# Performance work log

Measured on AMD Instinct MI355X. Metric: run time of the kernel, lower is better.

## Reference

```python
import jax, jax.numpy as jnp
import numpy as np
from jax import lax

C_LIGHT = 3e8
SPATIAL, CROP = 64, 128
BIN_LEN, WALL, SAMP_COEFF, CYCLES = 0.01, 2.0, 2.0, 5
B, D = 2, 1


def _waveconvparam(bin_resolution, virtual_wavelength, cycles):
    samples = int(round(cycles * virtual_wavelength / (C_LIGHT * bin_resolution)))
    num_cycles = samples * (C_LIGHT * bin_resolution) / virtual_wavelength
    sigma = 0.3
    g = np.arange(samples, dtype=np.float64)
    env = np.exp(-(((g - samples / 2.0) / (samples / 2.0)) ** 2) / (2 * sigma ** 2))
    cos_k = np.cos(2 * np.pi * num_cycles * g / samples) * env
    sin_k = np.sin(2 * np.pi * num_cycles * g / samples) * env
    return cos_k, sin_k


def _define_psf(N, M, slope):
    # LCT psf: locus of min |(4 slope)^2 (x^2+y^2) - z|, normalized and circularly shifted
    x = np.arange(2 * N, dtype=np.float64) / (2 * N - 1) * 2 - 1
    z = np.arange(2 * M, dtype=np.float64) / (2 * M - 1) * 2
    gy, gx, gz = np.meshgrid(x, x, z)  # (2N,2N,2M)
    blur = np.abs((4 * slope) ** 2 * (gx ** 2 + gy ** 2) - gz)
    d = (np.abs(blur - blur.min(axis=2, keepdims=True)) < 1e-8).astype(np.float64)
    e = d / np.sqrt(d.sum())
    f = np.roll(np.roll(e, N, axis=0), N, axis=1)
    return np.transpose(f, (2, 0, 1))  # (2M,2N,2N)


def _resampling_operator(M):
    row = M * M
    x = np.arange(1, row + 1, dtype=np.float64)
    mtx = np.zeros((row, M), dtype=np.float64)
    mtx[np.arange(row), np.ceil(np.sqrt(x)).astype(np.int64) - 1] = 1.0
    mtx = mtx / np.sqrt(x)[:, None]
    mtxi = mtx.T.copy()
    for _ in range(int(np.log2(M))):
        mtx = 0.5 * (mtx[0::2] + mtx[1::2])
        mtxi = 0.5 * (mtxi[:, 0::2] + mtxi[:, 1::2])
    return mtx.astype(np.float32), mtxi.astype(np.float32)


def setup_inputs() -> dict:
    key = jax.random.key(0)
    kf, kw, kb = jax.random.split(key, 3)
    bin_res = BIN_LEN / C_LIGHT
    trange = CROP * C_LIGHT * bin_res
    slope = (WALL / 2.0) / trange
    vlam = SAMP_COEFF * 2.0 * (WALL / (SPATIAL - 1))
    cos_k, sin_k = _waveconvparam(bin_res, vlam, CYCLES)
    wave = np.stack([cos_k, sin_k], 0)[:, ::-1][:, None, :].astype(np.float32)  # (2,1,k)
    psf = _define_psf(SPATIAL, CROP, slope)
    invpsf = np.conj(np.fft.fftn(psf))
    mtx, mtxi = _resampling_operator(CROP)
    return {
        "feature": jax.random.normal(kf, (B, D, CROP, SPATIAL, SPATIAL), jnp.float32),
        "conv_w": jax.random.normal(kw, ()) * 0.1 + 1.0,
        "conv_b": jax.random.normal(kb, ()) * 0.1,
        "wave": jnp.asarray(wave),
        "invpsf_real": jnp.asarray(np.real(invpsf).astype(np.float32))[None],
        "invpsf_imag": jnp.asarray(np.imag(invpsf).astype(np.float32))[None],
        "mtx": jnp.asarray(mtx),
        "mtxi": jnp.asarray(mtxi),
    }


def _attention(k1, k2, w, b):
    # SE-style cross attention; Conv3d(1,1,1) on unbatched (C=1,T,H,W) is w*x+b
    T = k2.shape[1]
    pe = jnp.sin(jnp.arange(T, dtype=k2.dtype))  # PE3D with 1 channel -> sin along T
    k2p = k2 + pe[None, :, None, None]
    scal = jnp.mean(w * k1 + b)  # conv + adaptive_avg_pool3d(1), channel dim = 1
    q = (w * k2p + b).reshape(1, 1, -1)
    attn = jax.nn.sigmoid(jax.nn.softmax(scal * q, axis=2)).reshape(k2p.shape)
    return attn * k2p


def _fre_atten2(kernel, w, b):
    _, T, H, W = kernel.shape
    ct, ch, cw = T // 2, H // 2, W // 2
    st, sh, sw = (T - ct) // 2, (H - ch) // 2, (W - cw) // 2
    sl = (slice(None), slice(ct - st, ct + st), slice(ch - sh, ch + sh), slice(cw - sw, cw + sw))
    high = kernel[sl]
    low = jnp.roll(kernel, (ct, ch, cw), axis=(1, 2, 3))[sl]
    l2l = _attention(low, low, w, b)
    l2h = _attention(l2l, high, w, b)
    temp = kernel.at[sl].set(l2h)
    temp = jnp.roll(temp, (ct, ch, cw), axis=(1, 2, 3)).at[sl].set(l2l)
    return jnp.roll(temp, (ct, ch, cw), axis=(1, 2, 3))


def _forward(feature, conv_w, conv_b, wave, invpsf_real, invpsf_imag, mtx, mtxi):
    b, d, T, H, W = feature.shape
    BD = b * d
    k = wave.shape[2]
    # virtual wave conv along time: (BDHW,1,T) x (2,1,k)
    data = feature.reshape(BD, T, H, W).transpose(0, 2, 3, 1).reshape(-1, 1, T)
    conv = lax.conv_general_dilated(data, wave, (1,), [(k // 2, k // 2)],
                                    dimension_numbers=("NCH", "OIH", "NCH"))
    if k % 2 == 0:
        conv = conv[:, :, 1:]
    data2 = conv.reshape(BD, H, W, 2, T).transpose(3, 0, 4, 1, 2).reshape(2 * BD, T, H, W)
    # temporal resampling then zero-pad to 2T,2H,2W
    tmp = jnp.einsum("tm,bmx->btx", mtx, data2.reshape(2 * BD, T, H * W)).reshape(2 * BD, T, H, W)
    datapad = jnp.zeros((2 * BD, 2 * T, 2 * H, 2 * W), feature.dtype).at[:, :T, :H, :W].set(tmp)
    datafre = jnp.fft.fftn(datapad)  # torch.fft.fftn transforms ALL dims incl. batch
    w1 = _fre_atten2(invpsf_real, conv_w, conv_b)
    w2 = _fre_atten2(invpsf_imag, conv_w, conv_b)
    re_real = datafre.real * w1 - datafre.imag * w2
    re_imag = datafre.real * w2 + datafre.imag * w1
    re = jnp.fft.ifftn(lax.complex(re_real, re_imag))
    vol = re[:, :T, :H, :W]
    cr, ci = vol[:BD].real, vol[:BD].imag
    sr, si = vol[BD:].real, vol[BD:].imag
    sum_real = cr ** 2 - ci ** 2 + sr ** 2 - si ** 2
    sum_imag = 2 * cr * ci + 2 * sr * si
    mag = jax.nn.relu((jnp.sqrt(sum_real ** 2 + sum_imag ** 2) + sum_real) * 0.5)
    sq = jnp.sqrt(mag)
    out = jnp.einsum("tm,bmx->btx", mtxi, sq.reshape(BD, T, H * W))
    return out.reshape(b, d, T, H, W)


def reference(feature, conv_w, conv_b, wave, invpsf_real, invpsf_imag, mtx, mtxi):
    return _forward(feature, conv_w, conv_b, wave, invpsf_real, invpsf_imag, mtx, mtxi)
```

## Files before the change

kernel.cpp:

```cpp
#include <hip/hip_runtime.h>

#define BLKE 524288
#define VOLE 4194304
#define TCROP 2097152
#define PI2 6.283185307179586476925286766559

__device__ __forceinline__ float2 cmulf(float2 a, float2 b){
  return make_float2(a.x*b.x - a.y*b.y, a.x*b.y + a.y*b.x);
}
__device__ __forceinline__ float waveSum(float v){
  #pragma unroll
  for (int o=32;o;o>>=1) v += __shfl_xor(v,o);
  return v;
}
__device__ __forceinline__ float waveMaxf(float v){
  #pragma unroll
  for (int o=32;o;o>>=1) v = fmaxf(v,__shfl_xor(v,o));
  return v;
}
__device__ __forceinline__ float waveMinf(float v){
  #pragma unroll
  for (int o=32;o;o>>=1) v = fminf(v,__shfl_xor(v,o));
  return v;
}

__device__ __forceinline__ void bcastReduce5(const float* __restrict__ pA, int kap,
    float& sum, float& mnl, float& mxl, float& mnh, float& mxh, float* sm ){
  int tid = threadIdx.x;
  const float* q = pA + kap*1280 + tid*5;
  float s = q[0], a = q[1], b = q[2], c = q[3], d = q[4];
  s = waveSum(s); a = waveMinf(a); b = waveMaxf(b); c = waveMinf(c); d = waveMaxf(d);
  if ((tid&63)==0){ int w = tid>>6; sm[w]=s; sm[4+w]=a; sm[8+w]=b; sm[12+w]=c; sm[16+w]=d; }
  __syncthreads();
  sum = sm[0]+sm[1]+sm[2]+sm[3];
  mnl = fminf(fminf(sm[4],sm[5]),fminf(sm[6],sm[7]));
  mxl = fmaxf(fmaxf(sm[8],sm[9]),fmaxf(sm[10],sm[11]));
  mnh = fminf(fminf(sm[12],sm[13]),fminf(sm[14],sm[15]));
  mxh = fmaxf(fmaxf(sm[16],sm[17]),fmaxf(sm[18],sm[19]));
}

__device__ __forceinline__ float bcastSum256(const float* __restrict__ p, float* sm ){
  int tid = threadIdx.x;
  float s = waveSum(p[tid]);
  if ((tid&63)==0) sm[tid>>6] = s;
  __syncthreads();
  return sm[0]+sm[1]+sm[2]+sm[3];
}

__global__ void __launch_bounds__(256) kD1(const float* __restrict__ mtx,
                                           const float* __restrict__ wave,
                                           float* __restrict__ M,
                                           const float* __restrict__ Kr,
                                           const float* __restrict__ Ki,
                                           float* __restrict__ Lw, float* __restrict__ Hw,
                                           float* __restrict__ pA){
  __shared__ float spe[128];
  __shared__ float sm[20];
  int bid = blockIdx.x;
  int tid = threadIdx.x;
  if (bid < 512){
    int kap = bid >> 8, bx = bid & 255;
    const float* K = kap ? Ki : Kr;
    if (tid < 128) spe[tid] = sinf((float)tid);
    __syncthreads();
    float sum=0.f, mnl=3.4e38f, mxl=-3.4e38f, mnh=3.4e38f, mxh=-3.4e38f;
    int base = bx*256 + tid;
    #pragma unroll
    for (int it = 0; it < 8; it++){
      int e = base + it*65536;
      int tau = e >> 12, rem = e & 4095, eta = rem >> 6, om = rem & 63;
      float pe = spe[tau];
      float lo = K[(size_t)((tau+192)&255)*16384 + ((eta+96)&127)*128 + ((om+96)&127)];
      float hi = K[(size_t)(tau+64)*16384 + (eta+32)*128 + (om+32)];
      sum += lo;
      float lp = lo+pe, hp = hi+pe;
      Lw[kap*BLKE + e] = lp;
      Hw[kap*BLKE + e] = hp;
      mnl=fminf(mnl,lp); mxl=fmaxf(mxl,lp);
      mnh=fminf(mnh,hp); mxh=fmaxf(mxh,hp);
    }
    sum = waveSum(sum); mnl=waveMinf(mnl); mxl=waveMaxf(mxl); mnh=waveMinf(mnh); mxh=waveMaxf(mxh);
    if ((tid&63)==0){ int w=tid>>6; sm[w]=sum; sm[4+w]=mnl; sm[8+w]=mxl; sm[12+w]=mnh; sm[16+w]=mxh; }
    __syncthreads();
    if (tid==0){
      float* o = pA + kap*1280 + bx*5;
      o[0] = sm[0]+sm[1]+sm[2]+sm[3];
      o[1] = fminf(fminf(sm[4],sm[5]),fminf(sm[6],sm[7]));
      o[2] = fmaxf(fmaxf(sm[8],sm[9]),fmaxf(sm[10],sm[11]));
      o[3] = fminf(fminf(sm[12],sm[13]),fminf(sm[14],sm[15]));
      o[4] = fmaxf(fmaxf(sm[16],sm[17]),fmaxf(sm[18],sm[19]));
    }
  } else {
    int idx = (bid-512)*256 + tid;
    int o = idx >> 14, r = idx & 16383;
    int t = r >> 7, s = r & 127;
    float acc = 0.f;
    int mlo = s-31; if (mlo < 0) mlo = 0;
    int mhi = s+31; if (mhi > 127) mhi = 127;
    for (int m = mlo; m <= mhi; m++) acc += mtx[t*128+m]*wave[o*63 + (s-m+31)];
    M[idx] = acc;
  }
}

__global__ void __launch_bounds__(256) kD2(const float* __restrict__ feat,
                                           const float* __restrict__ M,
                                           float* __restrict__ tmp,
                                           const float* __restrict__ pA,
                                           const float* __restrict__ Lw,
                                           float* __restrict__ pB,
                                           const float* cw, const float* cb){
  __shared__ __align__(16) char smem[16640];
  __shared__ float sm[20], smo[4];
  int bid = blockIdx.x;
  int tid = threadIdx.x;
  if (bid < 512){
    int kap = bid >> 8, bx = bid & 255;
    float sum,mnl,mxl,mnh,mxh;
    bcastReduce5(pA,kap,sum,mnl,mxl,mnh,mxh,sm);
    float w = cw[0], b = cb[0];
    float s1 = w*(sum*(1.0f/BLKE)) + b;
    float a1 = s1*w, c1 = s1*b;
    float mx = (a1>=0.f) ? a1*mxl+c1 : a1*mnl+c1;
    float acc = 0.f;
    int base = kap*BLKE + bx*256 + tid;
    #pragma unroll
    for (int it = 0; it < 8; it++){
      float lp = Lw[base + it*65536];
      acc += expf(a1*lp + c1 - mx);
    }
    acc = waveSum(acc);
    if ((tid&63)==0) smo[tid>>6] = acc;
    __syncthreads();
    if (tid==0) pB[kap*256 + bx] = smo[0]+smo[1]+smo[2]+smo[3];
  } else {
    int e = bid - 512;
    int b = e >> 8, tt = (e >> 6) & 3, xt = e & 63;
    float (*LF)[64] = (float(*)[64])smem;
    float (*LM)[32][33] = (float(*)[32][33])(smem + 8192);
    int xx = tid & 63, tq = tid >> 6;
    float acc0[8] = {}, acc1[8] = {};
    const float* fb = feat + (size_t)b*BLKE;
    for (int sb = 0; sb < 4; sb++){
      #pragma unroll
      for (int j = 0; j < 8; j++){
        int idx = tid + j*256; int s = idx >> 6, x = idx & 63;
        LF[s][x] = fb[(size_t)(sb*32+s)*4096 + xt*64 + x];
      }
      #pragma unroll
      for (int j = 0; j < 8; j++){
        int idx = tid + j*256; int o = idx >> 10, r = idx & 1023;
        int trow = r >> 5, s = r & 31;
        LM[o][trow][s] = M[o*16384 + (tt*32+trow)*128 + sb*32+s];
      }
      __syncthreads();
      for (int s = 0; s < 32; s++){
        float f = LF[s][xx];
        #pragma unroll
        for (int i = 0; i < 8; i++){
          acc0[i] += LM[0][tq*8+i][s]*f;
          acc1[i] += LM[1][tq*8+i][s]*f;
        }
      }
      __syncthreads();
    }
    #pragma unroll
    for (int i = 0; i < 8; i++){
      int t = tt*32 + tq*8 + i;
      tmp[(size_t)(0*2+b)*BLKE + (size_t)t*4096 + xt*64+xx] = acc0[i];
      tmp[(size_t)(1*2+b)*BLKE + (size_t)t*4096 + xt*64+xx] = acc1[i];
    }
  }
}

__global__ void __launch_bounds__(256) kD3(const float* __restrict__ tmp,
                                           float2* __restrict__ Z2,
                                           const float* __restrict__ pA,
                                           const float* __restrict__ pB,
                                           const float* __restrict__ Lw,
                                           float* __restrict__ pC,
                                           const float* cw, const float* cb){
  __shared__ __align__(16) char smem[8832];
  __shared__ float sm[20], smB[4], smo[4];
  int bid = blockIdx.x;
  int tid = threadIdx.x;
  if (bid < 512){
    int kap = bid >> 8, bx = bid & 255;
    float sum,mnl,mxl,mnh,mxh;
    bcastReduce5(pA,kap,sum,mnl,mxl,mnh,mxh,sm);
    float d1 = bcastSum256(pB + kap*256, smB);
    float w = cw[0], b = cb[0];
    float s1 = w*(sum*(1.0f/BLKE)) + b;
    float a1 = s1*w, c1 = s1*b;
    float mx = (a1>=0.f) ? a1*mxl+c1 : a1*mnl+c1;
    float invd = 1.0f/d1;
    float acc = 0.f;
    int base = kap*BLKE + bx*256 + tid;
    #pragma unroll
    for (int it = 0; it < 8; it++){
      float lp = Lw[base + it*65536];
      float p = expf(a1*lp + c1 - mx)*invd;
      acc += lp/(1.f + expf(-p));
    }
    acc = waveSum(acc);
    if ((tid&63)==0) smo[tid>>6] = acc;
    __syncthreads();
    if (tid==0) pC[kap*256 + bx] = smo[0]+smo[1]+smo[2]+smo[3];
  } else {
    int e = bid - 512;
    int b = e >> 11, bx = e & 2047;
    float2 (*bA)[130] = (float2(*)[130])smem;
    float2 (*bB)[130] = (float2(*)[130])(smem + 4160);
    float2* tw = (float2*)(smem + 8320);
    if (tid < 64){
      double ang = -PI2 * (double)tid / 128.0;
      tw[tid] = make_float2((float)cos(ang), (float)sin(ang));
    }
    int l = tid >> 6, lane = tid & 63;
    int line = bx*4 + l;
    int t = line >> 6, h = line & 63;
    const float* pc = tmp + (size_t)b*BLKE + (size_t)t*4096 + h*64;
    const float* ps = tmp + (size_t)(2+b)*BLKE + (size_t)t*4096 + h*64;
    bA[l][lane] = make_float2(pc[lane], ps[lane]);
    bA[l][lane+64] = make_float2(0.f, 0.f);
    __syncthreads();
    float2 (*src)[130] = bA, (*dst)[130] = bB;
    int m = 1;
    #pragma unroll
    for (int st = 0; st < 7; st++){
      int i = lane;
      int jm = i & ~(m-1);
      float2 a = src[l][i], b2 = src[l][i+64];
      float2 s = make_float2(a.x+b2.x, a.y+b2.y);
      float2 d = make_float2(a.x-b2.x, a.y-b2.y);
      dst[l][i+jm]   = s;
      dst[l][i+jm+m] = cmulf(d, tw[jm]);
      __syncthreads();
      float2 (*tp)[130] = src; src = dst; dst = tp;
      m <<= 1;
    }
    float2* outp = Z2 + (size_t)b*TCROP + (size_t)t*16384 + (size_t)h*128;
    outp[lane]    = src[l][lane];
    outp[lane+64] = src[l][lane+64];
  }
}

__global__ void __launch_bounds__(256) kD4(float2* __restrict__ Z2,
                                           const float* __restrict__ pA,
                                           const float* __restrict__ pC,
                                           const float* __restrict__ Hw,
                                           float* __restrict__ pD,
                                           const float* cw, const float* cb){
  __shared__ __align__(16) char smem[33792];
  __shared__ float sm[20], smC[4], smo[4];
  int bid = blockIdx.x;
  int tid = threadIdx.x;
  if (bid < 512){
    int kap = bid >> 8, bx = bid & 255;
    float sum,mnl,mxl,mnh,mxh;
    bcastReduce5(pA,kap,sum,mnl,mxl,mnh,mxh,sm);
    float sl2 = bcastSum256(pC + kap*256, smC);
    float w = cw[0], b = cb[0];
    float s2 = w*(sl2*(1.0f/BLKE)) + b;
    float a2 = s2*w, c2 = s2*b;
    float mx = (a2>=0.f) ? a2*mxh+c2 : a2*mnh+c2;
    float acc = 0.f;
    int base = kap*BLKE + bx*256 + tid;
    #pragma unroll
    for (int it = 0; it < 8; it++){
      float hp = Hw[base + it*65536];
      acc += expf(a2*hp + c2 - mx);
    }
    acc = waveSum(acc);
    if ((tid&63)==0) smo[tid>>6] = acc;
    __syncthreads();
    if (tid==0) pD[kap*256 + bx] = smo[0]+smo[1]+smo[2]+smo[3];
  } else {
    int e = bid - 512;
    int b = e >> 10, bx = e & 1023;
    float2 (*bA)[130] = (float2(*)[130])smem;
    float2 (*bB)[130] = (float2(*)[130])(smem + 16640);
    float2* tw = (float2*)(smem + 33280);
    if (tid < 64){
      double ang = -PI2 * (double)tid / 128.0;
      tw[tid] = make_float2((float)cos(ang), (float)sin(ang));
    }
    float2* Z = Z2 + (size_t)b*TCROP;
    int t = bx >> 3; int w0 = (bx & 7) << 4;
    size_t base = (size_t)t*16384 + w0;
    #pragma unroll
    for (int q = 0; q < 4; q++){
      int idx = q*256 + tid; int wl = idx & 15, hh = idx >> 4;
      bA[wl][hh] = Z[base + (size_t)hh*128 + wl];
      bA[wl][hh+64] = make_float2(0.f, 0.f);
    }
    __syncthreads();
    float2 (*src)[130] = bA, (*dst)[130] = bB;
    int m = 1;
    #pragma unroll
    for (int st = 0; st < 7; st++){
      #pragma unroll
      for (int q = 0; q < 4; q++){
        int g = q*256 + tid; int li = g >> 6; int i = g & 63;
        int jm = i & ~(m-1);
        float2 a = src[li][i], b2 = src[li][i+64];
        float2 s = make_float2(a.x+b2.x, a.y+b2.y);
        float2 d = make_float2(a.x-b2.x, a.y-b2.y);
        dst[li][i+jm]   = s;
        dst[li][i+jm+m] = cmulf(d, tw[jm]);
      }
      __syncthreads();
      float2 (*tp)[130] = src; src = dst; dst = tp;
      m <<= 1;
    }
    #pragma unroll
    for (int q = 0; q < 8; q++){
      int idx = q*256 + tid; int wl = idx & 15, hh = idx >> 4;
      Z[base + (size_t)hh*128 + wl] = src[wl][hh];
    }
  }
}

__device__ __forceinline__ float attnv(float v, float a, float c, float mx, float invd){
  float p = expf(a*v + c - mx)*invd;
  return v / (1.f + expf(-p));
}
__device__ __forceinline__ float2 wcAt(int t, int h, int w,
                                       const float* __restrict__ Kr, const float* __restrict__ Ki,
                                       const float* spe, const float* P){
  size_t off = (size_t)t*16384 + (size_t)h*128 + w;
  float kr = Kr[off], ki = Ki[off];
  bool center = (t>=64 && t<192) && (h>=32 && h<96) && (w>=32 && w<96);
  int tc = (t+64)&255, hc = (h+32)&127, wc = (w+32)&127;
  bool corner = (tc<128) && (hc<64) && (wc<64);
  float2 o;
  if (center){
    float pe = spe[t-64];
    o.x = attnv(kr+pe, P[4],  P[5],  P[6],  P[7]);
    o.y = attnv(ki+pe, P[12], P[13], P[14], P[15]);
  } else if (corner){
    float pe = spe[tc];
    o.x = attnv(kr+pe, P[0], P[1],  P[2],  P[3]);
    o.y = attnv(ki+pe, P[8], P[9],  P[10], P[11]);
  } else {
    o.x = kr; o.y = ki;
  }
  return o;
}

__global__ void __launch_bounds__(256) kWcF(const float* __restrict__ Kr,
                                            const float* __restrict__ Ki,
                                            const float* __restrict__ pA,
                                            const float* __restrict__ pB,
                                            const float* __restrict__ pC,
                                            const float* __restrict__ pD,
                                            const float* cw, const float* cb,
                                            float2* __restrict__ Wc){
  __shared__ float spe[128];
  __shared__ float P[16];
  __shared__ float sm[20], smB[4], smC[4], smD[4];
  int tid = threadIdx.x;
  if (tid < 128) spe[tid] = sinf((float)tid);
  for (int kap = 0; kap < 2; kap++){
    if (kap) __syncthreads();
    float sum,mnl,mxl,mnh,mxh;
    bcastReduce5(pA,kap,sum,mnl,mxl,mnh,mxh,sm);
    float d1  = bcastSum256(pB + kap*256, smB);
    float sl2 = bcastSum256(pC + kap*256, smC);
    float d2  = bcastSum256(pD + kap*256, smD);
    if (tid==0){
      float w = cw[0], b = cb[0];
      float s1 = w*(sum*(1.0f/BLKE)) + b;
      float a1 = s1*w, c1 = s1*b;
      float mx1 = (a1>=0.f) ? a1*mxl+c1 : a1*mnl+c1;
      float s2 = w*(sl2*(1.0f/BLKE)) + b;
      float a2 = s2*w, c2 = s2*b;
      float mx2 = (a2>=0.f) ? a2*mxh+c2 : a2*mnh+c2;
      float* Q = P + kap*8;
      Q[0]=a1; Q[1]=c1; Q[2]=mx1; Q[3]=1.0f/d1;
      Q[4]=a2; Q[5]=c2; Q[6]=mx2; Q[7]=1.0f/d2;
    }
  }
  __syncthreads();
  #pragma unroll
  for (int q = 0; q < 4; q++){
    int idx = blockIdx.x*1024 + q*256 + tid;
    int t = idx >> 14, r = idx & 16383, h = r >> 7, w = r & 127;
    Wc[idx] = wcAt(t, h, w, Kr, Ki, spe, P);
  }
}

__global__ void __launch_bounds__(256) kTfused(const float2* __restrict__ Z2,
                                               float2* __restrict__ U2,
                                               float2* __restrict__ V2,
                                               const float2* __restrict__ Wc){
  __shared__ float2 buf[16][259];
  __shared__ float2 tw[256];
  int tid = threadIdx.x;
  {
    double ang = -PI2 * (double)tid / 256.0;
    tw[tid] = make_float2((float)cos(ang), (float)sin(ang));
  }
  int b = blockIdx.y;
  int bid = blockIdx.x;
  int h = bid >> 3, w0 = (bid & 7) << 4;
  int wl = tid & 15, pq = tid >> 4;
  const float2* Z = Z2 + (size_t)b*TCROP;
  size_t gbase = (size_t)h*128 + w0 + wl;
  #pragma unroll
  for (int q = 0; q < 8; q++){
    int p = q*16 + pq;
    buf[wl][p] = Z[(size_t)p*16384 + gbase];
    buf[wl][p+128] = make_float2(0.f, 0.f);
  }
  __syncthreads();
  #pragma unroll
  for (int st = 0; st < 4; st++){
    const int Q = 64 >> (2*st);
    const int f = 1 << (2*st);
    #pragma unroll
    for (int it = 0; it < 4; it++){
      int u = pq + 16*it;
      int j = u & (Q-1);
      int seg = u >> (6 - 2*st);
      int base = (seg << (8 - 2*st)) + j;
      float2 a0 = buf[wl][base];
      float2 a1 = buf[wl][base+Q];
      float2 a2 = buf[wl][base+2*Q];
      float2 a3 = buf[wl][base+3*Q];
      float2 t0 = make_float2(a0.x+a2.x, a0.y+a2.y);
      float2 t1 = make_float2(a0.x-a2.x, a0.y-a2.y);
      float2 t2 = make_float2(a1.x+a3.x, a1.y+a3.y);
      float2 t3 = make_float2(a1.x-a3.x, a1.y-a3.y);
      float2 z0 = make_float2(t0.x+t2.x, t0.y+t2.y);
      float2 z2 = make_float2(t0.x-t2.x, t0.y-t2.y);
      float2 z1 = make_float2(t1.x+t3.y, t1.y-t3.x);
      float2 z3 = make_float2(t1.x-t3.y, t1.y+t3.x);
      buf[wl][base]     = z0;
      buf[wl][base+Q]   = cmulf(z1, tw[f*j]);
      buf[wl][base+2*Q] = cmulf(z2, tw[2*f*j]);
      buf[wl][base+3*Q] = cmulf(z3, tw[3*f*j]);
    }
    __syncthreads();
  }
  float2 rg[16];
  #pragma unroll
  for (int q = 0; q < 16; q++) rg[q] = buf[wl][q*16 + pq];
  #pragma unroll
  for (int q = 0; q < 16; q++){
    int p = q*16 + pq;
    int kt = ((p&3)<<6) | (((p>>2)&3)<<4) | (((p>>4)&3)<<2) | ((p>>6)&3);
    float2 wc = Wc[(size_t)kt*16384 + (size_t)h*128 + w0 + wl];
    buf[wl][p] = cmulf(rg[q], wc);
  }
  __syncthreads();
  #pragma unroll
  for (int st = 0; st < 4; st++){
    const int Q = 1 << (2*st);
    const int f = 64 >> (2*st);
    #pragma unroll
    for (int it = 0; it < 4; it++){
      int u = pq + 16*it;
      int j = u & (Q-1);
      int seg = u >> (2*st);
      int base = (seg << (2*st + 2)) + j;
      float2 w1 = tw[f*j], w2 = tw[2*f*j], w3 = tw[3*f*j];
      float2 a0 = buf[wl][base];
      float2 r1 = buf[wl][base+Q];
      float2 r2 = buf[wl][base+2*Q];
      float2 r3 = buf[wl][base+3*Q];
      float2 b1 = make_float2(r1.x*w1.x + r1.y*w1.y, r1.y*w1.x - r1.x*w1.y);
      float2 b2 = make_float2(r2.x*w2.x + r2.y*w2.y, r2.y*w2.x - r2.x*w2.y);
      float2 b3 = make_float2(r3.x*w3.x + r3.y*w3.y, r3.y*w3.x - r3.x*w3.y);
      float2 t0 = make_float2(a0.x+b2.x, a0.y+b2.y);
      float2 t1 = make_float2(a0.x-b2.x, a0.y-b2.y);
      float2 t2 = make_float2(b1.x+b3.x, b1.y+b3.y);
      float2 t3 = make_float2(b1.x-b3.x, b1.y-b3.y);
      buf[wl][base]     = make_float2(t0.x+t2.x, t0.y+t2.y);
      buf[wl][base+Q]   = make_float2(t1.x-t3.y, t1.y+t3.x);
      buf[wl][base+2*Q] = make_float2(t0.x-t2.x, t0.y-t2.y);
      buf[wl][base+3*Q] = make_float2(t1.x+t3.y, t1.y-t3.x);
    }
    __syncthreads();
  }
  float2* Uo = U2 + (size_t)b*TCROP;
  #pragma unroll
  for (int q = 0; q < 8; q++){
    int p = q*16 + pq;
    Uo[(size_t)p*16384 + gbase] = buf[wl][p];
  }
  #pragma unroll
  for (int q = 0; q < 16; q++){
    int p = q*16 + pq;
    int kt = ((p&3)<<6) | (((p>>2)&3)<<4) | (((p>>4)&3)<<2) | ((p>>6)&3);
    int tm = (256-kt)&255, hm = (128-h)&127, wm = (128-(w0+wl))&127;
    float2 wc = Wc[(size_t)tm*16384 + (size_t)hm*128 + wm];
    wc.y = -wc.y;
    buf[wl][p] = cmulf(rg[q], wc);
  }
  __syncthreads();
  #pragma unroll
  for (int st = 0; st < 4; st++){
    const int Q = 1 << (2*st);
    const int f = 64 >> (2*st);
    #pragma unroll
    for (int it = 0; it < 4; it++){
      int u = pq + 16*it;
      int j = u & (Q-1);
      int seg = u >> (2*st);
      int base = (seg << (2*st + 2)) + j;
      float2 w1 = tw[f*j], w2 = tw[2*f*j], w3 = tw[3*f*j];
      float2 a0 = buf[wl][base];
      float2 r1 = buf[wl][base+Q];
      float2 r2 = buf[wl][base+2*Q];
      float2 r3 = buf[wl][base+3*Q];
      float2 b1 = make_float2(r1.x*w1.x + r1.y*w1.y, r1.y*w1.x - r1.x*w1.y);
      float2 b2 = make_float2(r2.x*w2.x + r2.y*w2.y, r2.y*w2.x - r2.x*w2.y);
      float2 b3 = make_float2(r3.x*w3.x + r3.y*w3.y, r3.y*w3.x - r3.x*w3.y);
      float2 t0 = make_float2(a0.x+b2.x, a0.y+b2.y);
      float2 t1 = make_float2(a0.x-b2.x, a0.y-b2.y);
      float2 t2 = make_float2(b1.x+b3.x, b1.y+b3.y);
      float2 t3 = make_float2(b1.x-b3.x, b1.y-b3.y);
      buf[wl][base]     = make_float2(t0.x+t2.x, t0.y+t2.y);
      buf[wl][base+Q]   = make_float2(t1.x-t3.y, t1.y+t3.x);
      buf[wl][base+2*Q] = make_float2(t0.x-t2.x, t0.y-t2.y);
      buf[wl][base+3*Q] = make_float2(t1.x+t3.y, t1.y-t3.x);
    }
    __syncthreads();
  }
  float2* Vo = V2 + (size_t)b*TCROP;
  #pragma unroll
  for (int q = 0; q < 8; q++){
    int p = q*16 + pq;
    Vo[(size_t)p*16384 + gbase] = buf[wl][p];
  }
}

__global__ void __launch_bounds__(256) kHi(float2* __restrict__ U2, float2* __restrict__ V2){
  __shared__ float2 bA[16][130], bB[16][130], tw[64];
  int tid = threadIdx.x;
  if (tid < 64){
    double ang = PI2 * (double)tid / 128.0;
    tw[tid] = make_float2((float)cos(ang), (float)sin(ang));
  }
  float2* Z = (blockIdx.z ? V2 : U2) + (size_t)blockIdx.y*TCROP;
  int bid = blockIdx.x;
  int t = bid >> 3; int w0 = (bid & 7) << 4;
  size_t base = (size_t)t*16384 + w0;
  #pragma unroll
  for (int q = 0; q < 8; q++){
    int idx = q*256 + tid; int wl = idx & 15, hh = idx >> 4;
    bA[wl][hh] = Z[base + (size_t)hh*128 + wl];
  }
  __syncthreads();
  float2 (*src)[130] = bA, (*dst)[130] = bB;
  int m = 1;
  #pragma unroll
  for (int st = 0; st < 7; st++){
    #pragma unroll
    for (int q = 0; q < 4; q++){
      int g = q*256 + tid; int li = g >> 6; int i = g & 63;
      int jm = i & ~(m-1);
      float2 a = src[li][i], b2 = src[li][i+64];
      float2 s = make_float2(a.x+b2.x, a.y+b2.y);
      float2 d = make_float2(a.x-b2.x, a.y-b2.y);
      dst[li][i+jm]   = s;
      dst[li][i+jm+m] = cmulf(d, tw[jm]);
    }
    __syncthreads();
    float2 (*tp)[130] = src; src = dst; dst = tp;
    m <<= 1;
  }
  #pragma unroll
  for (int q = 0; q < 4; q++){
    int idx = q*256 + tid; int wl = idx & 15, hh = idx >> 4;
    Z[base + (size_t)hh*128 + wl] = src[wl][hh];
  }
}

__global__ void __launch_bounds__(256) kI3C(const float2* __restrict__ U2,
                                            const float2* __restrict__ V2,
                                            float* __restrict__ sq){
  __shared__ float2 bA[4][130], bB[4][130], tw[64];
  int tid = threadIdx.x;
  if (tid < 64){
    double ang = PI2 * (double)tid / 128.0;
    tw[tid] = make_float2((float)cos(ang), (float)sin(ang));
  }
  int b = blockIdx.y;
  int l = tid >> 6, lane = tid & 63;
  int line = blockIdx.x*4 + l;
  int t = line >> 6, h = line & 63;
  size_t off = (size_t)b*TCROP + (size_t)t*16384 + (size_t)h*128;
  bA[l][lane]    = U2[off + lane];
  bA[l][lane+64] = U2[off + lane + 64];
  __syncthreads();
  float2 (*src)[130] = bA, (*dst)[130] = bB;
  int m = 1;
  #pragma unroll
  for (int st = 0; st < 7; st++){
    int i = lane;
    int jm = i & ~(m-1);
    float2 a = src[l][i], b2 = src[l][i+64];
    float2 s = make_float2(a.x+b2.x, a.y+b2.y);
    float2 d = make_float2(a.x-b2.x, a.y-b2.y);
    dst[l][i+jm]   = s;
    dst[l][i+jm+m] = cmulf(d, tw[jm]);
    __syncthreads();
    float2 (*tp)[130] = src; src = dst; dst = tp;
    m <<= 1;
  }
  float2 y = src[l][lane];
  dst[l][lane]    = V2[off + lane];
  dst[l][lane+64] = V2[off + lane + 64];
  __syncthreads();
  src = dst; dst = (src == bA) ? bB : bA;
  m = 1;
  #pragma unroll
  for (int st = 0; st < 7; st++){
    int i = lane;
    int jm = i & ~(m-1);
    float2 a = src[l][i], b2 = src[l][i+64];
    float2 s = make_float2(a.x+b2.x, a.y+b2.y);
    float2 d = make_float2(a.x-b2.x, a.y-b2.y);
    dst[l][i+jm]   = s;
    dst[l][i+jm+m] = cmulf(d, tw[jm]);
    __syncthreads();
    float2 (*tp)[130] = src; src = dst; dst = tp;
    m <<= 1;
  }
  float2 v = src[l][lane];
  const float sc = 1.0f/(float)VOLE;
  const float sc2 = sc*sc;
  float2 s = cmulf(y, make_float2(v.x, -v.y));
  s.x *= sc2; s.y *= sc2;
  float mag = 0.5f*(sqrtf(s.x*s.x + s.y*s.y) + s.x);
  mag = fmaxf(mag, 0.f);
  sq[(size_t)b*BLKE + (size_t)t*4096 + h*64 + lane] = sqrtf(mag);
}

__global__ void __launch_bounds__(256) kOut(const float* __restrict__ sq,
                                            const float* __restrict__ mtxi,
                                            float* __restrict__ out){
  __shared__ float LF[32][64];
  __shared__ float LM[32][33];
  int b = blockIdx.z, tt = blockIdx.y, xt = blockIdx.x;
  int tid = threadIdx.x;
  int xx = tid & 63, tq = tid >> 6;
  float acc[8] = {};
  const float* fb = sq + (size_t)b*BLKE;
  for (int sb = 0; sb < 4; sb++){
    #pragma unroll
    for (int j = 0; j < 8; j++){
      int idx = tid + j*256; int s = idx >> 6, x = idx & 63;
      LF[s][x] = fb[(size_t)(sb*32+s)*4096 + xt*64 + x];
    }
    #pragma unroll
    for (int j = 0; j < 4; j++){
      int idx = tid + j*256; int trow = idx >> 5, s = idx & 31;
      LM[trow][s] = mtxi[(tt*32+trow)*128 + sb*32+s];
    }
    __syncthreads();
    for (int s = 0; s < 32; s++){
      float f = LF[s][xx];
      #pragma unroll
      for (int i = 0; i < 8; i++) acc[i] += LM[tq*8+i][s]*f;
    }
    __syncthreads();
  }
  #pragma unroll
  for (int i = 0; i < 8; i++){
    int t = tt*32 + tq*8 + i;
    out[(size_t)b*BLKE + (size_t)t*4096 + xt*64+xx] = acc[i];
  }
}

extern "C" void kernel_launch(void* const* d_in, const int* in_sizes, int n_in,
                              void* d_out, int out_size, void* d_ws, size_t ws_size,
                              hipStream_t stream){
  const float* feature = (const float*)d_in[0];
  const float* convW   = (const float*)d_in[1];
  const float* convB   = (const float*)d_in[2];
  const float* wave    = (const float*)d_in[3];
  const float* Kr      = (const float*)d_in[4];
  const float* Ki      = (const float*)d_in[5];
  const float* mtx     = (const float*)d_in[6];
  const float* mtxi    = (const float*)d_in[7];
  float* out = (float*)d_out;
  float* ws  = (float*)d_ws;

  float*  M    = ws;
  float*  pA   = ws + 32832;
  float*  pB   = ws + 35392;
  float*  pC   = ws + 35904;
  float*  pD   = ws + 36416;
  float*  tmp  = ws + 65536;
  float*  sq   = ws + 65536 + 2097152;
  float2* Z2   = (float2*)(ws + 3211264);
  float2* U2   = (float2*)(ws + 11599872);
  float2* V2   = (float2*)(ws + 19988480);
  float2* Wc   = (float2*)(ws + 28377088);
  float*  Lw   = (float*)U2;
  float*  Hw   = ((float*)U2) + 1048576;

  kD1 <<<640,  256, 0, stream>>>(mtx, wave, M, Kr, Ki, Lw, Hw, pA);
  kD2 <<<1024, 256, 0, stream>>>(feature, M, tmp, pA, Lw, pB, convW, convB);
  kD3 <<<4608, 256, 0, stream>>>(tmp, Z2, pA, pB, Lw, pC, convW, convB);
  kD4 <<<2560, 256, 0, stream>>>(Z2, pA, pC, Hw, pD, convW, convB);
  kWcF<<<4096, 256, 0, stream>>>(Kr, Ki, pA, pB, pC, pD, convW, convB, Wc);
  kTfused<<<dim3(1024,2), 256, 0, stream>>>(Z2, U2, V2, Wc);
  kHi<<<dim3(1024,2,2), 256, 0, stream>>>(U2, V2);
  kI3C<<<dim3(2048,2), 256, 0, stream>>>(U2, V2, sq);
  kOut<<<dim3(64,4,2), 256, 0, stream>>>(sq, mtxi, out);
}
```

Before: 276.9 us.

## Fuse weight computation into T-FFT kernel, precompute twiddles, widen blocks to 512

Removes the kWcF kernel that materialized the full frequency-domain weight volume Wc, and instead computes the weights on the fly inside kTfused from Kr/Ki and a small parameter block produced by a new single-block kP kernel. Twiddle tables are computed once in an extra kD1 block and loaded from global memory by the FFT kernels instead of being recomputed in double precision per block. kTfused and kHi move to 512-thread blocks with half the per-thread work. This trades a large write and re-read of Wc for extra per-element weight arithmetic and scattered Kr/Ki reads inside the FFT kernel, and adds a tiny serial launch.

```diff
diff --git a/kernel.cpp b/kernel.cpp
--- a/kernel.cpp
+++ b/kernel.cpp
@@ -53,7 +53,10 @@
                                            const float* __restrict__ Kr,
                                            const float* __restrict__ Ki,
                                            float* __restrict__ Lw, float* __restrict__ Hw,
-                                           float* __restrict__ pA){
+                                           float* __restrict__ pA,
+                                           float2* __restrict__ twF,
+                                           float2* __restrict__ twD,
+                                           float2* __restrict__ twI){
   __shared__ float spe[128];
   __shared__ float sm[20];
   int bid = blockIdx.x;
@@ -90,7 +93,7 @@
       o[3] = fminf(fminf(sm[12],sm[13]),fminf(sm[14],sm[15]));
       o[4] = fmaxf(fmaxf(sm[16],sm[17]),fmaxf(sm[18],sm[19]));
     }
-  } else {
+  } else if (bid < 640){
     int idx = (bid-512)*256 + tid;
     int o = idx >> 14, r = idx & 16383;
     int t = r >> 7, s = r & 127;
@@ -99,6 +102,17 @@
     int mhi = s+31; if (mhi > 127) mhi = 127;
     for (int m = mlo; m <= mhi; m++) acc += mtx[t*128+m]*wave[o*63 + (s-m+31)];
     M[idx] = acc;
+  } else {
+    if (tid < 256){
+      double ang = -PI2 * (double)tid / 256.0;
+      twF[tid] = make_float2((float)cos(ang), (float)sin(ang));
+    }
+    if (tid < 64){
+      double a2 = -PI2 * (double)tid / 128.0;
+      twD[tid] = make_float2((float)cos(a2), (float)sin(a2));
+      double a3 =  PI2 * (double)tid / 128.0;
+      twI[tid] = make_float2((float)cos(a3), (float)sin(a3));
+    }
   }
 }
 
@@ -178,7 +192,8 @@
                                            const float* __restrict__ pB,
                                            const float* __restrict__ Lw,
                                            float* __restrict__ pC,
-                                           const float* cw, const float* cb){
+                                           const float* cw, const float* cb,
+                                           const float2* __restrict__ twg){
   __shared__ __align__(16) char smem[8832];
   __shared__ float sm[20], smB[4], smo[4];
   int bid = blockIdx.x;
@@ -211,10 +226,7 @@
     float2 (*bA)[130] = (float2(*)[130])smem;
     float2 (*bB)[130] = (float2(*)[130])(smem + 4160);
     float2* tw = (float2*)(smem + 8320);
-    if (tid < 64){
-      double ang = -PI2 * (double)tid / 128.0;
-      tw[tid] = make_float2((float)cos(ang), (float)sin(ang));
-    }
+    if (tid < 64) tw[tid] = twg[tid];
     int l = tid >> 6, lane = tid & 63;
     int line = bx*4 + l;
     int t = line >> 6, h = line & 63;
@@ -249,7 +261,8 @@
                                            const float* __restrict__ pC,
                                            const float* __restrict__ Hw,
                                            float* __restrict__ pD,
-                                           const float* cw, const float* cb){
+                                           const float* cw, const float* cb,
+                                           const float2* __restrict__ twg){
   __shared__ __align__(16) char smem[33792];
   __shared__ float sm[20], smC[4], smo[4];
   int bid = blockIdx.x;
@@ -280,10 +293,7 @@
     float2 (*bA)[130] = (float2(*)[130])smem;
     float2 (*bB)[130] = (float2(*)[130])(smem + 16640);
     float2* tw = (float2*)(smem + 33280);
-    if (tid < 64){
-      double ang = -PI2 * (double)tid / 128.0;
-      tw[tid] = make_float2((float)cos(ang), (float)sin(ang));
-    }
+    if (tid < 64) tw[tid] = twg[tid];
     float2* Z = Z2 + (size_t)b*TCROP;
     int t = bx >> 3; int w0 = (bx & 7) << 4;
     size_t base = (size_t)t*16384 + w0;
@@ -347,19 +357,14 @@
   return o;
 }
 
-__global__ void __launch_bounds__(256) kWcF(const float* __restrict__ Kr,
-                                            const float* __restrict__ Ki,
-                                            const float* __restrict__ pA,
-                                            const float* __restrict__ pB,
-                                            const float* __restrict__ pC,
-                                            const float* __restrict__ pD,
-                                            const float* cw, const float* cb,
-                                            float2* __restrict__ Wc){
-  __shared__ float spe[128];
-  __shared__ float P[16];
+__global__ void __launch_bounds__(256) kP(const float* __restrict__ pA,
+                                          const float* __restrict__ pB,
+                                          const float* __restrict__ pC,
+                                          const float* __restrict__ pD,
+                                          const float* cw, const float* cb,
+                                          float* __restrict__ Pg){
   __shared__ float sm[20], smB[4], smC[4], smD[4];
   int tid = threadIdx.x;
-  if (tid < 128) spe[tid] = sinf((float)tid);
   for (int kap = 0; kap < 2; kap++){
     if (kap) __syncthreads();
     float sum,mnl,mxl,mnh,mxh;
@@ -375,31 +380,28 @@
       float s2 = w*(sl2*(1.0f/BLKE)) + b;
       float a2 = s2*w, c2 = s2*b;
       float mx2 = (a2>=0.f) ? a2*mxh+c2 : a2*mnh+c2;
-      float* Q = P + kap*8;
+      float* Q = Pg + kap*8;
       Q[0]=a1; Q[1]=c1; Q[2]=mx1; Q[3]=1.0f/d1;
       Q[4]=a2; Q[5]=c2; Q[6]=mx2; Q[7]=1.0f/d2;
     }
   }
-  __syncthreads();
-  #pragma unroll
-  for (int q = 0; q < 4; q++){
-    int idx = blockIdx.x*1024 + q*256 + tid;
-    int t = idx >> 14, r = idx & 16383, h = r >> 7, w = r & 127;
-    Wc[idx] = wcAt(t, h, w, Kr, Ki, spe, P);
-  }
-}
-
-__global__ void __launch_bounds__(256) kTfused(const float2* __restrict__ Z2,
-                                               float2* __restrict__ U2,
-                                               float2* __restrict__ V2,
-                                               const float2* __restrict__ Wc){
+}
+
+__global__ void __launch_bounds__(512,8) kTfused(const float2* __restrict__ Z2,
+                                                 float2* __restrict__ U2,
+                                                 float2* __restrict__ V2,
+                                                 const float* __restrict__ Kr,
+                                                 const float* __restrict__ Ki,
+                                                 const float* __restrict__ Pg,
+                                                 const float2* __restrict__ twg){
   __shared__ float2 buf[16][259];
   __shared__ float2 tw[256];
-  int tid = threadIdx.x;
-  {
-    double ang = -PI2 * (double)tid / 256.0;
-    tw[tid] = make_float2((float)cos(ang), (float)sin(ang));
-  }
+  __shared__ float spe[128];
+  __shared__ float P[16];
+  int tid = threadIdx.x;
+  if (tid < 256) tw[tid] = twg[tid];
+  else if (tid < 384) spe[tid-256] = sinf((float)(tid-256));
+  else if (tid < 400) P[tid-384] = Pg[tid-384];
   int b = blockIdx.y;
   int bid = blockIdx.x;
   int h = bid >> 3, w0 = (bid & 7) << 4;
@@ -407,8 +409,8 @@
   const float2* Z = Z2 + (size_t)b*TCROP;
   size_t gbase = (size_t)h*128 + w0 + wl;
   #pragma unroll
-  for (int q = 0; q < 8; q++){
-    int p = q*16 + pq;
+  for (int q = 0; q < 4; q++){
+    int p = q*32 + pq;
     buf[wl][p] = Z[(size_t)p*16384 + gbase];
     buf[wl][p+128] = make_float2(0.f, 0.f);
   }
@@ -418,8 +420,8 @@
     const int Q = 64 >> (2*st);
     const int f = 1 << (2*st);
     #pragma unroll
-    for (int it = 0; it < 4; it++){
-      int u = pq + 16*it;
+    for (int it = 0; it < 2; it++){
+      int u = pq + 32*it;
       int j = u & (Q-1);
       int seg = u >> (6 - 2*st);
       int base = (seg << (8 - 2*st)) + j;
@@ -442,14 +444,14 @@
     }
     __syncthreads();
   }
-  float2 rg[16];
-  #pragma unroll
-  for (int q = 0; q < 16; q++) rg[q] = buf[wl][q*16 + pq];
-  #pragma unroll
-  for (int q = 0; q < 16; q++){
-    int p = q*16 + pq;
+  float2 rg[8];
+  #pragma unroll
+  for (int q = 0; q < 8; q++) rg[q] = buf[wl][q*32 + pq];
+  #pragma unroll
+  for (int q = 0; q < 8; q++){
+    int p = q*32 + pq;
     int kt = ((p&3)<<6) | (((p>>2)&3)<<4) | (((p>>4)&3)<<2) | ((p>>6)&3);
-    float2 wc = Wc[(size_t)kt*16384 + (size_t)h*128 + w0 + wl];
+    float2 wc = wcAt(kt, h, w0 + wl, Kr, Ki, spe, P);
     buf[wl][p] = cmulf(rg[q], wc);
   }
   __syncthreads();
@@ -458,8 +460,8 @@
     const int Q = 1 << (2*st);
     const int f = 64 >> (2*st);
     #pragma unroll
-    for (int it = 0; it < 4; it++){
-      int u = pq + 16*it;
+    for (int it = 0; it < 2; it++){
+      int u = pq + 32*it;
       int j = u & (Q-1);
       int seg = u >> (2*st);
       int base = (seg << (2*st + 2)) + j;
@@ -484,16 +486,16 @@
   }
   float2* Uo = U2 + (size_t)b*TCROP;
   #pragma unroll
+  for (int q = 0; q < 4; q++){
+    int p = q*32 + pq;
+    Uo[(size_t)p*16384 + gbase] = buf[wl][p];
+  }
+  #pragma unroll
   for (int q = 0; q < 8; q++){
-    int p = q*16 + pq;
-    Uo[(size_t)p*16384 + gbase] = buf[wl][p];
-  }
-  #pragma unroll
-  for (int q = 0; q < 16; q++){
-    int p = q*16 + pq;
+    int p = q*32 + pq;
     int kt = ((p&3)<<6) | (((p>>2)&3)<<4) | (((p>>4)&3)<<2) | ((p>>6)&3);
     int tm = (256-kt)&255, hm = (128-h)&127, wm = (128-(w0+wl))&127;
-    float2 wc = Wc[(size_t)tm*16384 + (size_t)hm*128 + wm];
+    float2 wc = wcAt(tm, hm, wm, Kr, Ki, spe, P);
     wc.y = -wc.y;
     buf[wl][p] = cmulf(rg[q], wc);
   }
@@ -503,8 +505,8 @@
     const int Q = 1 << (2*st);
     const int f = 64 >> (2*st);
     #pragma unroll
-    for (int it = 0; it < 4; it++){
-      int u = pq + 16*it;
+    for (int it = 0; it < 2; it++){
+      int u = pq + 32*it;
       int j = u & (Q-1);
       int seg = u >> (2*st);
       int base = (seg << (2*st + 2)) + j;
@@ -529,26 +531,24 @@
   }
   float2* Vo = V2 + (size_t)b*TCROP;
   #pragma unroll
-  for (int q = 0; q < 8; q++){
-    int p = q*16 + pq;
+  for (int q = 0; q < 4; q++){
+    int p = q*32 + pq;
     Vo[(size_t)p*16384 + gbase] = buf[wl][p];
   }
 }
 
-__global__ void __launch_bounds__(256) kHi(float2* __restrict__ U2, float2* __restrict__ V2){
+__global__ void __launch_bounds__(512,8) kHi(float2* __restrict__ U2, float2* __restrict__ V2,
+                                             const float2* __restrict__ twg){
   __shared__ float2 bA[16][130], bB[16][130], tw[64];
   int tid = threadIdx.x;
-  if (tid < 64){
-    double ang = PI2 * (double)tid / 128.0;
-    tw[tid] = make_float2((float)cos(ang), (float)sin(ang));
-  }
+  if (tid < 64) tw[tid] = twg[tid];
   float2* Z = (blockIdx.z ? V2 : U2) + (size_t)blockIdx.y*TCROP;
   int bid = blockIdx.x;
   int t = bid >> 3; int w0 = (bid & 7) << 4;
   size_t base = (size_t)t*16384 + w0;
   #pragma unroll
-  for (int q = 0; q < 8; q++){
-    int idx = q*256 + tid; int wl = idx & 15, hh = idx >> 4;
+  for (int q = 0; q < 4; q++){
+    int idx = q*512 + tid; int wl = idx & 15, hh = idx >> 4;
     bA[wl][hh] = Z[base + (size_t)hh*128 + wl];
   }
   __syncthreads();
@@ -557,8 +557,8 @@
   #pragma unroll
   for (int st = 0; st < 7; st++){
     #pragma unroll
-    for (int q = 0; q < 4; q++){
-      int g = q*256 + tid; int li = g >> 6; int i = g & 63;
+    for (int q = 0; q < 2; q++){
+      int g = q*512 + tid; int li = g >> 6; int i = g & 63;
       int jm = i & ~(m-1);
       float2 a = src[li][i], b2 = src[li][i+64];
       float2 s = make_float2(a.x+b2.x, a.y+b2.y);
@@ -571,21 +571,19 @@
     m <<= 1;
   }
   #pragma unroll
-  for (int q = 0; q < 4; q++){
-    int idx = q*256 + tid; int wl = idx & 15, hh = idx >> 4;
+  for (int q = 0; q < 2; q++){
+    int idx = q*512 + tid; int wl = idx & 15, hh = idx >> 4;
     Z[base + (size_t)hh*128 + wl] = src[wl][hh];
   }
 }
 
 __global__ void __launch_bounds__(256) kI3C(const float2* __restrict__ U2,
                                             const float2* __restrict__ V2,
-                                            float* __restrict__ sq){
+                                            float* __restrict__ sq,
+                                            const float2* __restrict__ twg){
   __shared__ float2 bA[4][130], bB[4][130], tw[64];
   int tid = threadIdx.x;
-  if (tid < 64){
-    double ang = PI2 * (double)tid / 128.0;
-    tw[tid] = make_float2((float)cos(ang), (float)sin(ang));
-  }
+  if (tid < 64) tw[tid] = twg[tid];
   int b = blockIdx.y;
   int l = tid >> 6, lane = tid & 63;
   int line = blockIdx.x*4 + l;
@@ -693,22 +691,25 @@
   float*  pB   = ws + 35392;
   float*  pC   = ws + 35904;
   float*  pD   = ws + 36416;
+  float*  Pg   = ws + 37440;
+  float2* twF  = (float2*)(ws + 40960);
+  float2* twD  = (float2*)(ws + 41472);
+  float2* twI  = (float2*)(ws + 41600);
   float*  tmp  = ws + 65536;
   float*  sq   = ws + 65536 + 2097152;
   float2* Z2   = (float2*)(ws + 3211264);
   float2* U2   = (float2*)(ws + 11599872);
   float2* V2   = (float2*)(ws + 19988480);
-  float2* Wc   = (float2*)(ws + 28377088);
   float*  Lw   = (float*)U2;
   float*  Hw   = ((float*)U2) + 1048576;
 
-  kD1 <<<640,  256, 0, stream>>>(mtx, wave, M, Kr, Ki, Lw, Hw, pA);
+  kD1 <<<641,  256, 0, stream>>>(mtx, wave, M, Kr, Ki, Lw, Hw, pA, twF, twD, twI);
   kD2 <<<1024, 256, 0, stream>>>(feature, M, tmp, pA, Lw, pB, convW, convB);
-  kD3 <<<4608, 256, 0, stream>>>(tmp, Z2, pA, pB, Lw, pC, convW, convB);
-  kD4 <<<2560, 256, 0, stream>>>(Z2, pA, pC, Hw, pD, convW, convB);
-  kWcF<<<4096, 256, 0, stream>>>(Kr, Ki, pA, pB, pC, pD, convW, convB, Wc);
-  kTfused<<<dim3(1024,2), 256, 0, stream>>>(Z2, U2, V2, Wc);
-  kHi<<<dim3(1024,2,2), 256, 0, stream>>>(U2, V2);
-  kI3C<<<dim3(2048,2), 256, 0, stream>>>(U2, V2, sq);
+  kD3 <<<4608, 256, 0, stream>>>(tmp, Z2, pA, pB, Lw, pC, convW, convB, twD);
+  kD4 <<<2560, 256, 0, stream>>>(Z2, pA, pC, Hw, pD, convW, convB, twD);
+  kP  <<<1,    256, 0, stream>>>(pA, pB, pC, pD, convW, convB, Pg);
+  kTfused<<<dim3(1024,2), 512, 0, stream>>>(Z2, U2, V2, Kr, Ki, Pg, twF);
+  kHi<<<dim3(1024,2,2), 512, 0, stream>>>(U2, V2, twI);
+  kI3C<<<dim3(2048,2), 256, 0, stream>>>(U2, V2, sq, twI);
   kOut<<<dim3(64,4,2), 256, 0, stream>>>(sq, mtxi, out);
 }
```

Result: slower. 300.2 us (+8.4%).
